# Kernel optimization log

Measured on AMD Instinct MI355X. Metric: run time of the kernel, lower is better.

Reference implementation:

```python
import jax, jax.numpy as jnp
import numpy as np

B, T = 2, 1023
C, H, HS, L, FF = 1024, 16, 64, 6, 4096
V, BS = 50258, 1024


def setup_inputs() -> dict:
    key = jax.random.key(0)
    ks = iter(jax.random.split(key, 80))
    def w(shape):
        return 0.02 * jax.random.normal(next(ks), shape, dtype=jnp.float32)
    inp = {}
    inp['x'] = jax.random.randint(next(ks), (B, T), 0, V)
    inp['y'] = jax.random.randint(next(ks), (B, T), 0, V)
    inp['wte'] = w((V, C))
    inp['wpe_x'] = w((BS, C))
    inp['wpe_y'] = w((BS, C))
    # encoder blocks (stacked over L layers)
    inp['enc_Wq'] = w((L, H, C, HS)); inp['enc_Wk'] = w((L, H, C, HS)); inp['enc_Wv'] = w((L, H, C, HS))
    inp['enc_pw'] = w((L, C, C)); inp['enc_pb'] = jnp.zeros((L, C), jnp.float32)
    inp['enc_ln1g'] = jnp.ones((L, C), jnp.float32); inp['enc_ln1b'] = jnp.zeros((L, C), jnp.float32)
    inp['enc_ln2g'] = jnp.ones((L, C), jnp.float32); inp['enc_ln2b'] = jnp.zeros((L, C), jnp.float32)
    inp['enc_w1'] = w((L, C, FF)); inp['enc_b1'] = jnp.zeros((L, FF), jnp.float32)
    inp['enc_w2'] = w((L, FF, C)); inp['enc_b2'] = jnp.zeros((L, C), jnp.float32)
    # decoder blocks: self-attn (masked), cross-attn, ffn
    inp['dec_sWq'] = w((L, H, C, HS)); inp['dec_sWk'] = w((L, H, C, HS)); inp['dec_sWv'] = w((L, H, C, HS))
    inp['dec_spw'] = w((L, C, C)); inp['dec_spb'] = jnp.zeros((L, C), jnp.float32)
    inp['dec_cWq'] = w((L, H, C, HS)); inp['dec_cWk'] = w((L, H, C, HS)); inp['dec_cWv'] = w((L, H, C, HS))
    inp['dec_cpw'] = w((L, C, C)); inp['dec_cpb'] = jnp.zeros((L, C), jnp.float32)
    inp['dec_ln1g'] = jnp.ones((L, C), jnp.float32); inp['dec_ln1b'] = jnp.zeros((L, C), jnp.float32)
    inp['dec_ln2g'] = jnp.ones((L, C), jnp.float32); inp['dec_ln2b'] = jnp.zeros((L, C), jnp.float32)
    inp['dec_ln3g'] = jnp.ones((L, C), jnp.float32); inp['dec_ln3b'] = jnp.zeros((L, C), jnp.float32)
    inp['dec_w1'] = w((L, C, FF)); inp['dec_b1'] = jnp.zeros((L, FF), jnp.float32)
    inp['dec_w2'] = w((L, FF, C)); inp['dec_b2'] = jnp.zeros((L, C), jnp.float32)
    inp['lnf_g'] = jnp.ones((C,), jnp.float32); inp['lnf_b'] = jnp.zeros((C,), jnp.float32)
    inp['lm_b'] = jnp.zeros((V,), jnp.float32)  # lm_head weight tied to wte
    return inp


def _ln(x, g, b):
    m = x.mean(-1, keepdims=True)
    v = ((x - m) ** 2).mean(-1, keepdims=True)
    return g * (x - m) / jnp.sqrt(v + 1e-5) + b


def _mha(xq, xkv, Wq, Wk, Wv, pw, pb, causal):
    # per-head projections batched over heads: [B,T,C] x [H,C,HS] -> [B,H,T,HS]
    q = jnp.einsum('btc,hcd->bhtd', xq, Wq)
    k = jnp.einsum('bsc,hcd->bhsd', xkv, Wk)
    v = jnp.einsum('bsc,hcd->bhsd', xkv, Wv)
    # NOTE: original scales by sqrt(n_embed) (C from x.size()), not sqrt(head_size)
    s = jnp.einsum('bhtd,bhsd->bhts', q, k) / jnp.sqrt(jnp.float32(C))
    if causal:
        mask = jnp.tril(jnp.ones((xq.shape[1], xkv.shape[1]), bool))
        s = jnp.where(mask, s, -jnp.inf)
    a = jax.nn.softmax(s, axis=-1)
    o = jnp.einsum('bhts,bhsd->bhtd', a, v)
    o = o.transpose(0, 2, 1, 3).reshape(xq.shape[0], xq.shape[1], H * HS)
    return o @ pw + pb


def _ffn(x, w1, b1, w2, b2):
    return jnp.maximum(x @ w1 + b1, 0.0) @ w2 + b2


def _forward(x, y, p):
    enc = p['wte'][x] + p['wpe_x'][:x.shape[1]]
    for i in range(L):
        enc = enc + _ln(_mha(enc, enc, p['enc_Wq'][i], p['enc_Wk'][i], p['enc_Wv'][i], p['enc_pw'][i], p['enc_pb'][i], False), p['enc_ln1g'][i], p['enc_ln1b'][i])
        enc = enc + _ln(_ffn(enc, p['enc_w1'][i], p['enc_b1'][i], p['enc_w2'][i], p['enc_b2'][i]), p['enc_ln2g'][i], p['enc_ln2b'][i])
    dec = p['wte'][y] + p['wpe_y'][:y.shape[1]]
    for i in range(L):
        dec = dec + _ln(_mha(dec, dec, p['dec_sWq'][i], p['dec_sWk'][i], p['dec_sWv'][i], p['dec_spw'][i], p['dec_spb'][i], True), p['dec_ln1g'][i], p['dec_ln1b'][i])
        dec = dec + _ln(_mha(dec, enc, p['dec_cWq'][i], p['dec_cWk'][i], p['dec_cWv'][i], p['dec_cpw'][i], p['dec_cpb'][i], False), p['dec_ln2g'][i], p['dec_ln2b'][i])
        dec = dec + _ln(_ffn(dec, p['dec_w1'][i], p['dec_b1'][i], p['dec_w2'][i], p['dec_b2'][i]), p['dec_ln3g'][i], p['dec_ln3b'][i])
    dec = _ln(dec, p['lnf_g'], p['lnf_b'])
    return dec @ p['wte'].T + p['lm_b']


def reference(x, y, wte, wpe_x, wpe_y,
              enc_Wq, enc_Wk, enc_Wv, enc_pw, enc_pb, enc_ln1g, enc_ln1b, enc_ln2g, enc_ln2b,
              enc_w1, enc_b1, enc_w2, enc_b2,
              dec_sWq, dec_sWk, dec_sWv, dec_spw, dec_spb,
              dec_cWq, dec_cWk, dec_cWv, dec_cpw, dec_cpb,
              dec_ln1g, dec_ln1b, dec_ln2g, dec_ln2b, dec_ln3g, dec_ln3b,
              dec_w1, dec_b1, dec_w2, dec_b2,
              lnf_g, lnf_b, lm_b):
    p = dict(wte=wte, wpe_x=wpe_x, wpe_y=wpe_y,
             enc_Wq=enc_Wq, enc_Wk=enc_Wk, enc_Wv=enc_Wv, enc_pw=enc_pw, enc_pb=enc_pb,
             enc_ln1g=enc_ln1g, enc_ln1b=enc_ln1b, enc_ln2g=enc_ln2g, enc_ln2b=enc_ln2b,
             enc_w1=enc_w1, enc_b1=enc_b1, enc_w2=enc_w2, enc_b2=enc_b2,
             dec_sWq=dec_sWq, dec_sWk=dec_sWk, dec_sWv=dec_sWv, dec_spw=dec_spw, dec_spb=dec_spb,
             dec_cWq=dec_cWq, dec_cWk=dec_cWk, dec_cWv=dec_cWv, dec_cpw=dec_cpw, dec_cpb=dec_cpb,
             dec_ln1g=dec_ln1g, dec_ln1b=dec_ln1b, dec_ln2g=dec_ln2g, dec_ln2b=dec_ln2b,
             dec_ln3g=dec_ln3g, dec_ln3b=dec_ln3b,
             dec_w1=dec_w1, dec_b1=dec_b1, dec_w2=dec_w2, dec_b2=dec_b2,
             lnf_g=lnf_g, lnf_b=lnf_b, lm_b=lm_b)
    return _forward(x, y, p)
```

## Files before the change

### kernel.cpp

```cpp
#include <hip/hip_runtime.h>
#include <hip/hip_bf16.h>

#define BB 2
#define TT 1023
#define CC 1024
#define HH 16
#define HSZ 64
#define LL 6
#define FFD 4096
#define VV 50258
#define MM (BB*TT)
#define MP 2048
#define VP 50304

typedef __attribute__((ext_vector_type(4))) float  f32x4;
typedef __attribute__((ext_vector_type(8))) short  s16x8;
typedef __attribute__((ext_vector_type(4))) short  s16x4;

#define SCHED0   __builtin_amdgcn_sched_barrier(0)
#define SBAR     __builtin_amdgcn_s_barrier()
#define LGKMCNT0 asm volatile("s_waitcnt lgkmcnt(0)" ::: "memory")

__device__ __forceinline__ short f2b(float x) {
    __hip_bfloat16 h = __float2bfloat16(x);
    short s;
    __builtin_memcpy(&s, &h, 2);
    return s;
}
__device__ __forceinline__ float b2f(short s) {
    unsigned u = ((unsigned)(unsigned short)s) << 16;
    float f;
    __builtin_memcpy(&f, &u, 4);
    return f;
}

__device__ __forceinline__ void gld16(const void* g, void* l) {
    __builtin_amdgcn_global_load_lds(
        (__attribute__((address_space(1))) const void*)g,
        (__attribute__((address_space(3))) void*)l, 16, 0, 0);
}

__global__ __launch_bounds__(256) void embed_kernel(
    const int* __restrict__ ids, const float* __restrict__ wte,
    const float* __restrict__ wpe, float* __restrict__ out,
    __hip_bfloat16* __restrict__ outb)
{
    int r = blockIdx.x;
    int t = r % TT;
    long id = ids[r];
    int c = threadIdx.x * 4;
    float4 a = *(const float4*)(wte + id * (long)CC + c);
    float4 p = *(const float4*)(wpe + (long)t * CC + c);
    float4 o; o.x = a.x + p.x; o.y = a.y + p.y; o.z = a.z + p.z; o.w = a.w + p.w;
    *(float4*)(out + (long)r * CC + c) = o;
    s16x4 h; h[0] = f2b(o.x); h[1] = f2b(o.y); h[2] = f2b(o.z); h[3] = f2b(o.w);
    *(s16x4*)(outb + (long)r * CC + c) = h;
}

__global__ __launch_bounds__(256) void cvtb_kernel(
    const float* __restrict__ in, __hip_bfloat16* __restrict__ out, long n)
{
    long i = ((long)blockIdx.x * 256 + threadIdx.x) * 8;
    if (i >= n) return;
    float4 f0 = *(const float4*)(in + i);
    float4 f1 = *(const float4*)(in + i + 4);
    s16x8 h;
    h[0]=f2b(f0.x); h[1]=f2b(f0.y); h[2]=f2b(f0.z); h[3]=f2b(f0.w);
    h[4]=f2b(f1.x); h[5]=f2b(f1.y); h[6]=f2b(f1.z); h[7]=f2b(f1.w);
    *(s16x8*)(out + i) = h;
}

__global__ __launch_bounds__(256) void tcvt_kernel(
    const float* __restrict__ in, __hip_bfloat16* __restrict__ out,
    int R, int S, long inZ, long outZa, long outZb, int zdiv)
{
    int z = blockIdx.z;
    in  += (long)z * inZ;
    out += (long)(z / zdiv) * outZa + (long)(z % zdiv) * outZb;
    __shared__ float tile[32][33];
    int s0 = blockIdx.x * 32, r0 = blockIdx.y * 32;
    int tx = threadIdx.x, ty = threadIdx.y;
    #pragma unroll
    for (int i = 0; i < 4; ++i)
        tile[ty + i * 8][tx] = in[(long)(r0 + ty + i * 8) * S + s0 + tx];
    __syncthreads();
    #pragma unroll
    for (int i = 0; i < 4; ++i)
        out[(long)(s0 + ty + i * 8) * R + r0 + tx] =
            __float2bfloat16(tile[tx][ty + i * 8]);
}

template<int WMODE, bool RELU, int BM, int BN>
__global__ __launch_bounds__(256) void mgemm2_kernel(
    const __hip_bfloat16* __restrict__ A, const __hip_bfloat16* __restrict__ B,
    const float* __restrict__ bias, float* __restrict__ Cm,
    __hip_bfloat16* __restrict__ Cb,
    int M, int N, int K, int ldc, int GM)
{
    constexpr int ASZ  = BM * 32;
    constexpr int BSZ  = BN * 32;
    constexpr int BUF  = ASZ + BSZ;
    constexpr int WROW = BM / 2;
    constexpr int WCOL = BN / 2;
    constexpr int NI   = WROW / 16;
    constexpr int NJ   = WCOL / 16;
    constexpr int NAC  = BM / 64;
    constexpr int NBC  = BN / 64;
    constexpr int L    = NAC + NBC;
    __shared__ short LDS[3 * BUF];

    const int nwg = gridDim.x;
    const int bid = blockIdx.x;
    const int q = nwg >> 3, r = nwg & 7;
    const int xcd = bid & 7, lid = bid >> 3;
    const int swz = (xcd < r) ? xcd * (q + 1) + lid
                              : r * (q + 1) + (xcd - r) * q + lid;
    const int m0 = (swz % GM) * BM;
    const int n0 = (swz / GM) * BN;

    const int tid  = threadIdx.x;
    const int lane = tid & 63, w = tid >> 6;
    const int wr = w >> 1, wc = w & 1;
    const int lr = lane & 15, kg = lane >> 4;

    const __hip_bfloat16* Abase = A + (long)m0 * K;
    const __hip_bfloat16* Bbase = B + (long)n0 * K;

    f32x4 acc[NI][NJ];
    #pragma unroll
    for (int i = 0; i < NI; ++i)
        #pragma unroll
        for (int j = 0; j < NJ; ++j)
            acc[i][j] = (f32x4){0.f, 0.f, 0.f, 0.f};

    const int srow = lane >> 2;
    const int scol = (((lane & 3) ^ ((lane >> 3) & 3))) * 8;

    auto stage = [&](int db, long kofs) {
        short* Ad = &LDS[db * BUF];
        short* Bd = Ad + ASZ;
        #pragma unroll
        for (int p = 0; p < NAC; ++p) {
            int cc = p * 4 + w;
            long ro = (long)(cc * 16 + srow) * K + kofs + scol;
            gld16(Abase + ro, Ad + cc * 512);
        }
        #pragma unroll
        for (int p = 0; p < NBC; ++p) {
            int cc = p * 4 + w;
            long ro = (long)(cc * 16 + srow) * K + kofs + scol;
            gld16(Bbase + ro, Bd + cc * 512);
        }
    };
    const int rslot = (kg ^ ((lr >> 1) & 3)) * 8;

    auto compute = [&](int db) {
        const short* Ar = &LDS[db * BUF];
        const short* Br = Ar + ASZ;
        s16x8 af[NI], bf[NJ];
        #pragma unroll
        for (int i = 0; i < NI; ++i)
            af[i] = *(const s16x8*)&Ar[(wr * WROW + i * 16 + lr) * 32 + rslot];
        #pragma unroll
        for (int j = 0; j < NJ; ++j)
            bf[j] = *(const s16x8*)&Br[(wc * WCOL + j * 16 + lr) * 32 + rslot];
        __builtin_amdgcn_s_setprio(1);
        #pragma unroll
        for (int i = 0; i < NI; ++i)
            #pragma unroll
            for (int j = 0; j < NJ; ++j)
                acc[i][j] = __builtin_amdgcn_mfma_f32_16x16x32_bf16(
                    af[i], bf[j], acc[i][j], 0, 0, 0);
        __builtin_amdgcn_s_setprio(0);
    };

    const int nt = K >> 5;
    stage(0, 0);
    if (nt > 1) stage(1, 32);
    int db = 0;
    for (int t = 0; t < nt; ++t) {
        if (t + 2 < nt) {
            stage((db + 2) % 3, (long)(t + 2) << 5);
            SCHED0;
            if constexpr (L == 4) asm volatile("s_waitcnt vmcnt(8)" ::: "memory");
            else asm volatile("s_waitcnt vmcnt(6)" ::: "memory");
            SCHED0;
        } else if (t + 1 < nt) {
            SCHED0;
            if constexpr (L == 4) asm volatile("s_waitcnt vmcnt(4)" ::: "memory");
            else asm volatile("s_waitcnt vmcnt(3)" ::: "memory");
            SCHED0;
        } else {
            SCHED0; asm volatile("s_waitcnt vmcnt(0)" ::: "memory"); SCHED0;
        }
        SBAR; SCHED0;
        compute(db);
        SCHED0; LGKMCNT0; SCHED0; SBAR; SCHED0;
        db = (db + 1) % 3;
    }

    if (WMODE == 0) {
        float* LF = (float*)&LDS[0];
        if (BM == 128) {
            #pragma unroll
            for (int h = 0; h < 2; ++h) {
                if (wc == h) {
                    #pragma unroll
                    for (int j = 0; j < NJ; ++j) {
                        int gcol = n0 + h * WCOL + j * 16 + lr;
                        float bv = (bias && gcol < N) ? bias[gcol] : 0.f;
                        #pragma unroll
                        for (int i = 0; i < NI; ++i) {
                            int row0 = wr * WROW + i * 16 + kg * 4;
                            #pragma unroll
                            for (int qq = 0; qq < 4; ++qq) {
                                float v = acc[i][j][qq] + bv;
                                if (RELU) v = fmaxf(v, 0.f);
                                LF[(row0 + qq) * 64 + j * 16 + lr] = v;
                            }
                        }
                    }
                }
                __syncthreads();
                #pragma unroll
                for (int i = 0; i < 16; ++i) {
                    int F = i * 256 + tid;
                    int row = F >> 5, col = (F & 31) * 2;
                    int gr = m0 + row, gc = n0 + h * 64 + col;
                    if (gr < M && gc < N)
                        *(float2*)(Cm + (long)gr * ldc + gc) = *(const float2*)&LF[row * 64 + col];
                }
                __syncthreads();
            }
        } else {
            #pragma unroll
            for (int j = 0; j < NJ; ++j) {
                int gcol = n0 + wc * WCOL + j * 16 + lr;
                float bv = (bias && gcol < N) ? bias[gcol] : 0.f;
                #pragma unroll
                for (int i = 0; i < NI; ++i) {
                    int row0 = wr * WROW + i * 16 + kg * 4;
                    #pragma unroll
                    for (int qq = 0; qq < 4; ++qq) {
                        float v = acc[i][j][qq] + bv;
                        if (RELU) v = fmaxf(v, 0.f);
                        LF[(row0 + qq) * BN + wc * WCOL + j * 16 + lr] = v;
                    }
                }
            }
            __syncthreads();
            #pragma unroll
            for (int i = 0; i < BM * BN / 512; ++i) {
                int F = i * 256 + tid;
                int row = F / (BN / 2), col = (F % (BN / 2)) * 2;
                int gr = m0 + row, gc = n0 + col;
                if (gr < M && gc < N)
                    *(float2*)(Cm + (long)gr * ldc + gc) = *(const float2*)&LF[row * BN + col];
            }
        }
    } else {
        short* LS = (short*)&LDS[0];
        #pragma unroll
        for (int j = 0; j < NJ; ++j) {
            int gcol = n0 + wc * WCOL + j * 16 + lr;
            float bv = (bias && gcol < N) ? bias[gcol] : 0.f;
            #pragma unroll
            for (int i = 0; i < NI; ++i) {
                int row0 = wr * WROW + i * 16 + kg * 4;
                #pragma unroll
                for (int qq = 0; qq < 4; ++qq) {
                    float v = acc[i][j][qq] + bv;
                    if (RELU) v = fmaxf(v, 0.f);
                    LS[(row0 + qq) * BN + wc * WCOL + j * 16 + lr] = f2b(v);
                }
            }
        }
        __syncthreads();
        #pragma unroll
        for (int i = 0; i < BM * BN / 2048; ++i) {
            int F = i * 256 + tid;
            int row = F / (BN / 8), col = (F % (BN / 8)) * 8;
            int gr = m0 + row, gc = n0 + col;
            if (gr < M && gc < N)
                *(s16x8*)((short*)Cb + (long)gr * ldc + gc) = *(const s16x8*)&LS[row * BN + col];
        }
    }
}

__global__ __launch_bounds__(256) void mgemm_f32b_kernel(
    const float* __restrict__ A, const float* __restrict__ Bv,
    const float* __restrict__ bias, float* __restrict__ Cm,
    int M, int N, int K, int ldc)
{
    __shared__ short As[128][40];
    __shared__ short Bs[128][40];
    const int tid  = threadIdx.x;
    const int lane = tid & 63, w = tid >> 6;
    const int wr = w >> 1, wc = w & 1;
    const int lr = lane & 15, kg = lane >> 4;
    const int m0 = blockIdx.y * 128, n0 = blockIdx.x * 128;
    const int ar = tid >> 3, ac = (tid & 7) * 4;
    const int br = tid >> 2, bc = (tid & 3) * 8;

    f32x4 acc[4][4];
    #pragma unroll
    for (int i = 0; i < 4; ++i)
        #pragma unroll
        for (int j = 0; j < 4; ++j)
            acc[i][j] = (f32x4){0.f, 0.f, 0.f, 0.f};

    for (int k0 = 0; k0 < K; k0 += 32) {
        #pragma unroll
        for (int p = 0; p < 4; ++p) {
            int row = ar + p * 32, gm = m0 + row;
            float4 f = {0.f, 0.f, 0.f, 0.f};
            if (gm < M) f = *(const float4*)(A + (long)gm * K + k0 + ac);
            s16x4 h; h[0] = f2b(f.x); h[1] = f2b(f.y); h[2] = f2b(f.z); h[3] = f2b(f.w);
            *(s16x4*)&As[row][ac] = h;
        }
        #pragma unroll
        for (int p = 0; p < 2; ++p) {
            int n = br + p * 64, gn = n0 + n;
            s16x8 h = (s16x8){0,0,0,0,0,0,0,0};
            if (gn < N) {
                float4 f0 = *(const float4*)(Bv + (long)gn * K + k0 + bc);
                float4 f1 = *(const float4*)(Bv + (long)gn * K + k0 + bc + 4);
                h[0]=f2b(f0.x); h[1]=f2b(f0.y); h[2]=f2b(f0.z); h[3]=f2b(f0.w);
                h[4]=f2b(f1.x); h[5]=f2b(f1.y); h[6]=f2b(f1.z); h[7]=f2b(f1.w);
            }
            *(s16x8*)&Bs[n][bc] = h;
        }
        __syncthreads();
        s16x8 af[4], bf[4];
        #pragma unroll
        for (int i = 0; i < 4; ++i) af[i] = *(const s16x8*)&As[wr*64 + i*16 + lr][kg*8];
        #pragma unroll
        for (int j = 0; j < 4; ++j) bf[j] = *(const s16x8*)&Bs[wc*64 + j*16 + lr][kg*8];
        #pragma unroll
        for (int i = 0; i < 4; ++i)
            #pragma unroll
            for (int j = 0; j < 4; ++j)
                acc[i][j] = __builtin_amdgcn_mfma_f32_16x16x32_bf16(af[i], bf[j], acc[i][j], 0, 0, 0);
        __syncthreads();
    }
    #pragma unroll
    for (int j = 0; j < 4; ++j) {
        int gcol = n0 + wc * 64 + j * 16 + lr;
        if (gcol >= N) continue;
        float bv = bias ? bias[gcol] : 0.f;
        #pragma unroll
        for (int i = 0; i < 4; ++i) {
            int grow0 = m0 + wr * 64 + i * 16 + kg * 4;
            #pragma unroll
            for (int qq = 0; qq < 4; ++qq) {
                int gr = grow0 + qq;
                if (gr >= M) continue;
                Cm[(long)gr * ldc + gcol] = acc[i][j][qq] + bv;
            }
        }
    }
}

template<bool CAUSAL>
__global__ __launch_bounds__(256) void fattn_kernel(
    const __hip_bfloat16* __restrict__ qkvb, __hip_bfloat16* __restrict__ outb)
{
    __shared__ short Ks[128][72];
    __shared__ short Vt[64][136];
    __shared__ short Ps[4][16][136];

    const int q0 = blockIdx.x * 64;
    const int h = blockIdx.y, b = blockIdx.z;
    const int tid = threadIdx.x;
    const int lane = tid & 63, w = tid >> 6;
    const int lr = lane & 15, lg = lane >> 4;

    const long base = (long)b * TT * 3072;
    const __hip_bfloat16* Kg = qkvb + base + 1024 + h * 64;
    const __hip_bfloat16* Vg = qkvb + base + 2048 + h * 64;

    s16x8 qf[2];
    {
        int qr = q0 + w * 16 + lr;
        #pragma unroll
        for (int kc = 0; kc < 2; ++kc) {
            s16x8 hv = (s16x8){0,0,0,0,0,0,0,0};
            if (qr < TT) {
                hv = *(const s16x8*)(qkvb + base + (long)qr * 3072 + h * 64 + kc * 32 + lg * 8);
                #pragma unroll
                for (int e = 0; e < 8; ++e)
                    hv[e] = f2b(b2f(hv[e]) * 0.03125f);
            }
            qf[kc] = hv;
        }
    }

    f32x4 acc[4];
    #pragma unroll
    for (int jd = 0; jd < 4; ++jd) acc[jd] = (f32x4){0.f, 0.f, 0.f, 0.f};
    float mrun[4] = {-3.0e38f, -3.0e38f, -3.0e38f, -3.0e38f};
    float lrun[4] = {0.f, 0.f, 0.f, 0.f};

    const int send = CAUSAL ? min(TT, q0 + 64) : TT;
    const int nt = (send + 127) >> 7;
    const int sr4 = (tid >> 3) * 4;
    const int dcc = (tid & 7) * 8;

    s16x8 kreg[4], vreg[4];
    auto loadkv = [&](int t) {
        int sbase = t * 128;
        #pragma unroll
        for (int rr = 0; rr < 4; ++rr) {
            int sg = sbase + sr4 + rr;
            if (sg < TT) {
                kreg[rr] = *(const s16x8*)(Kg + (long)sg * 3072 + dcc);
                vreg[rr] = *(const s16x8*)(Vg + (long)sg * 3072 + dcc);
            } else {
                kreg[rr] = (s16x8){0,0,0,0,0,0,0,0};
                vreg[rr] = (s16x8){0,0,0,0,0,0,0,0};
            }
        }
    };

    loadkv(0);
    for (int ti = 0; ti < nt; ++ti) {
        const int s0 = ti * 128;
        SCHED0; SBAR; SCHED0;
        #pragma unroll
        for (int rr = 0; rr < 4; ++rr)
            *(s16x8*)&Ks[sr4 + rr][dcc] = kreg[rr];
        #pragma unroll
        for (int pr = 0; pr < 2; ++pr) {
            #pragma unroll
            for (int e = 0; e < 8; ++e) {
                unsigned pack = (unsigned)(unsigned short)vreg[2*pr][e]
                              | ((unsigned)(unsigned short)vreg[2*pr + 1][e] << 16);
                *(unsigned*)&Vt[dcc + e][sr4 + 2*pr] = pack;
            }
        }
        if (ti + 1 < nt) loadkv(ti + 1);
        SCHED0; LGKMCNT0; SCHED0; SBAR; SCHED0;

        f32x4 sf[8];
        __builtin_amdgcn_s_setprio(1);
        #pragma unroll
        for (int j = 0; j < 8; ++j) {
            f32x4 z = (f32x4){0.f, 0.f, 0.f, 0.f};
            #pragma unroll
            for (int kc = 0; kc < 2; ++kc) {
                s16x8 kf = *(const s16x8*)&Ks[j * 16 + lr][kc * 32 + lg * 8];
                z = __builtin_amdgcn_mfma_f32_16x16x32_bf16(qf[kc], kf, z, 0, 0, 0);
            }
            sf[j] = z;
        }
        __builtin_amdgcn_s_setprio(0);

        float mloc[4] = {-3.0e38f, -3.0e38f, -3.0e38f, -3.0e38f};
        #pragma unroll
        for (int j = 0; j < 8; ++j) {
            int sg = s0 + j * 16 + lr;
            #pragma unroll
            for (int r = 0; r < 4; ++r) {
                float sc = sf[j][r];
                int qg = q0 + w * 16 + lg * 4 + r;
                if ((CAUSAL && sg > qg) || sg >= TT) sc = -3.0e38f;
                sf[j][r] = sc;
                mloc[r] = fmaxf(mloc[r], sc);
            }
        }
        #pragma unroll
        for (int r = 0; r < 4; ++r)
            #pragma unroll
            for (int off = 1; off < 16; off <<= 1)
                mloc[r] = fmaxf(mloc[r], __shfl_xor(mloc[r], off));

        bool grow = false;
        #pragma unroll
        for (int r = 0; r < 4; ++r)
            grow = grow || (mloc[r] > mrun[r] + 8.0f);
        if (__any((int)grow)) {
            #pragma unroll
            for (int r = 0; r < 4; ++r) {
                float mn = fmaxf(mrun[r], mloc[r]);
                float corr = __expf(mrun[r] - mn);
                mrun[r] = mn;
                lrun[r] *= corr;
                #pragma unroll
                for (int jd = 0; jd < 4; ++jd) acc[jd][r] *= corr;
            }
        }

        float psum[4] = {0.f, 0.f, 0.f, 0.f};
        #pragma unroll
        for (int j = 0; j < 8; ++j) {
            #pragma unroll
            for (int r = 0; r < 4; ++r) {
                float p = __expf(sf[j][r] - mrun[r]);
                psum[r] += p;
                Ps[w][lg * 4 + r][j * 16 + lr] = f2b(p);
            }
        }
        #pragma unroll
        for (int r = 0; r < 4; ++r) {
            #pragma unroll
            for (int off = 1; off < 16; off <<= 1)
                psum[r] += __shfl_xor(psum[r], off);
            lrun[r] += psum[r];
        }

        __builtin_amdgcn_s_setprio(1);
        #pragma unroll
        for (int kc = 0; kc < 4; ++kc) {
            s16x8 pa = *(const s16x8*)&Ps[w][lr][kc * 32 + lg * 8];
            #pragma unroll
            for (int jd = 0; jd < 4; ++jd) {
                s16x8 bv = *(const s16x8*)&Vt[jd * 16 + lr][kc * 32 + lg * 8];
                acc[jd] = __builtin_amdgcn_mfma_f32_16x16x32_bf16(pa, bv, acc[jd], 0, 0, 0);
            }
        }
        __builtin_amdgcn_s_setprio(0);
        SCHED0; LGKMCNT0; SCHED0;
    }

    #pragma unroll
    for (int r = 0; r < 4; ++r) {
        int qg = q0 + w * 16 + lg * 4 + r;
        if (qg >= TT) continue;
        float inv = 1.0f / lrun[r];
        #pragma unroll
        for (int jd = 0; jd < 4; ++jd)
            outb[((long)b * TT + qg) * CC + h * 64 + jd * 16 + lr] =
                __float2bfloat16(acc[jd][r] * inv);
    }
}

__global__ __launch_bounds__(256) void ln_kernel(
    const float* __restrict__ in, const float* __restrict__ res,
    const float* __restrict__ g, const float* __restrict__ b,
    float* __restrict__ out, __hip_bfloat16* __restrict__ outb)
{
    const int r = blockIdx.x, tid = threadIdx.x;
    __shared__ float sm[4];

    float4 xv = *(const float4*)(in + (long)r * CC + tid * 4);
    float s = xv.x + xv.y + xv.z + xv.w;
    #pragma unroll
    for (int o = 32; o > 0; o >>= 1) s += __shfl_xor(s, o);
    if ((tid & 63) == 0) sm[tid >> 6] = s;
    __syncthreads();
    const float mean = (sm[0] + sm[1] + sm[2] + sm[3]) * (1.0f / CC);
    __syncthreads();

    float4 d; d.x = xv.x - mean; d.y = xv.y - mean; d.z = xv.z - mean; d.w = xv.w - mean;
    float s2 = d.x * d.x + d.y * d.y + d.z * d.z + d.w * d.w;
    #pragma unroll
    for (int o = 32; o > 0; o >>= 1) s2 += __shfl_xor(s2, o);
    if ((tid & 63) == 0) sm[tid >> 6] = s2;
    __syncthreads();
    const float rstd = rsqrtf((sm[0] + sm[1] + sm[2] + sm[3]) * (1.0f / CC) + 1e-5f);

    float4 gv = *(const float4*)(g + tid * 4);
    float4 bv = *(const float4*)(b + tid * 4);
    float4 o;
    o.x = gv.x * d.x * rstd + bv.x; o.y = gv.y * d.y * rstd + bv.y;
    o.z = gv.z * d.z * rstd + bv.z; o.w = gv.w * d.w * rstd + bv.w;
    if (res) {
        float4 rv = *(const float4*)(res + (long)r * CC + tid * 4);
        o.x += rv.x; o.y += rv.y; o.z += rv.z; o.w += rv.w;
    }
    if (out) *(float4*)(out + (long)r * CC + tid * 4) = o;
    if (outb) {
        s16x4 h; h[0] = f2b(o.x); h[1] = f2b(o.y); h[2] = f2b(o.z); h[3] = f2b(o.w);
        *(s16x4*)(outb + (long)r * CC + tid * 4) = h;
    }
}

__global__ __launch_bounds__(256) void lnb_kernel(
    const __hip_bfloat16* __restrict__ in, const float* __restrict__ res,
    const float* __restrict__ g, const float* __restrict__ b,
    float* __restrict__ out, __hip_bfloat16* __restrict__ outb)
{
    const int r = blockIdx.x, tid = threadIdx.x;
    __shared__ float sm[4];

    s16x4 hv = *(const s16x4*)((const short*)in + (long)r * CC + tid * 4);
    float4 xv;
    xv.x = b2f(hv[0]); xv.y = b2f(hv[1]); xv.z = b2f(hv[2]); xv.w = b2f(hv[3]);
    float s = xv.x + xv.y + xv.z + xv.w;
    #pragma unroll
    for (int o = 32; o > 0; o >>= 1) s += __shfl_xor(s, o);
    if ((tid & 63) == 0) sm[tid >> 6] = s;
    __syncthreads();
    const float mean = (sm[0] + sm[1] + sm[2] + sm[3]) * (1.0f / CC);
    __syncthreads();

    float4 d; d.x = xv.x - mean; d.y = xv.y - mean; d.z = xv.z - mean; d.w = xv.w - mean;
    float s2 = d.x * d.x + d.y * d.y + d.z * d.z + d.w * d.w;
    #pragma unroll
    for (int o = 32; o > 0; o >>= 1) s2 += __shfl_xor(s2, o);
    if ((tid & 63) == 0) sm[tid >> 6] = s2;
    __syncthreads();
    const float rstd = rsqrtf((sm[0] + sm[1] + sm[2] + sm[3]) * (1.0f / CC) + 1e-5f);

    float4 gv = *(const float4*)(g + tid * 4);
    float4 bv = *(const float4*)(b + tid * 4);
    float4 o;
    o.x = gv.x * d.x * rstd + bv.x; o.y = gv.y * d.y * rstd + bv.y;
    o.z = gv.z * d.z * rstd + bv.z; o.w = gv.w * d.w * rstd + bv.w;
    if (res) {
        float4 rv = *(const float4*)(res + (long)r * CC + tid * 4);
        o.x += rv.x; o.y += rv.y; o.z += rv.z; o.w += rv.w;
    }
    *(float4*)(out + (long)r * CC + tid * 4) = o;
    s16x4 hh; hh[0] = f2b(o.x); hh[1] = f2b(o.y); hh[2] = f2b(o.z); hh[3] = f2b(o.w);
    *(s16x4*)((short*)outb + (long)r * CC + tid * 4) = hh;
}

extern "C" void kernel_launch(void* const* d_in, const int* in_sizes, int n_in,
                              void* d_out, int out_size, void* d_ws, size_t ws_size,
                              hipStream_t stream)
{
    const int*   x      = (const int*)  d_in[0];
    const int*   y      = (const int*)  d_in[1];
    const float* wte    = (const float*)d_in[2];
    const float* wpe_x  = (const float*)d_in[3];
    const float* wpe_y  = (const float*)d_in[4];
    const float* eWq    = (const float*)d_in[5];
    const float* eWk    = (const float*)d_in[6];
    const float* eWv    = (const float*)d_in[7];
    const float* epw    = (const float*)d_in[8];
    const float* epb    = (const float*)d_in[9];
    const float* eln1g  = (const float*)d_in[10];
    const float* eln1b  = (const float*)d_in[11];
    const float* eln2g  = (const float*)d_in[12];
    const float* eln2b  = (const float*)d_in[13];
    const float* ew1    = (const float*)d_in[14];
    const float* eb1    = (const float*)d_in[15];
    const float* ew2    = (const float*)d_in[16];
    const float* eb2    = (const float*)d_in[17];
    const float* dsWq   = (const float*)d_in[18];
    const float* dsWk   = (const float*)d_in[19];
    const float* dsWv   = (const float*)d_in[20];
    const float* dspw   = (const float*)d_in[21];
    const float* dspb   = (const float*)d_in[22];
    const float* dcWq   = (const float*)d_in[23];
    const float* dcWk   = (const float*)d_in[24];
    const float* dcWv   = (const float*)d_in[25];
    const float* dcpw   = (const float*)d_in[26];
    const float* dcpb   = (const float*)d_in[27];
    const float* dln1g  = (const float*)d_in[28];
    const float* dln1b  = (const float*)d_in[29];
    const float* dln2g  = (const float*)d_in[30];
    const float* dln2b  = (const float*)d_in[31];
    const float* dln3g  = (const float*)d_in[32];
    const float* dln3b  = (const float*)d_in[33];
    const float* dw1    = (const float*)d_in[34];
    const float* db1    = (const float*)d_in[35];
    const float* dw2    = (const float*)d_in[36];
    const float* db2    = (const float*)d_in[37];
    const float* lnfg   = (const float*)d_in[38];
    const float* lnfb   = (const float*)d_in[39];
    const float* lm_b   = (const float*)d_in[40];

    float* out = (float*)d_out;

    const size_t MCp = (size_t)MP * CC;
    float* enc = (float*)d_ws;
    float* dec = enc + MCp;
    float* t0  = dec + MCp;
    __hip_bfloat16* encb = (__hip_bfloat16*)(t0 + MCp);
    __hip_bfloat16* decb = encb + MCp;
    __hip_bfloat16* t0b  = decb + MCp;
    __hip_bfloat16* a0b  = t0b + MCp;
    __hip_bfloat16* qkvb = a0b + MCp;
    __hip_bfloat16* ffb  = qkvb + (size_t)MP * 3072;
    __hip_bfloat16* wteb = ffb + (size_t)MP * FFD;
    __hip_bfloat16* eQKVw = wteb + (size_t)VP * CC;
    __hip_bfloat16* ePWw  = eQKVw + (size_t)LL * 3072 * CC;
    __hip_bfloat16* eW1w  = ePWw  + (size_t)LL * CC * CC;
    __hip_bfloat16* eW2w  = eW1w  + (size_t)LL * FFD * CC;
    __hip_bfloat16* sQKVw = eW2w  + (size_t)LL * CC * FFD;
    __hip_bfloat16* sPWw  = sQKVw + (size_t)LL * 3072 * CC;
    __hip_bfloat16* cQKVw = sPWw  + (size_t)LL * CC * CC;
    __hip_bfloat16* cPWw  = cQKVw + (size_t)LL * 3072 * CC;
    __hip_bfloat16* dW1w  = cPWw  + (size_t)LL * CC * CC;
    __hip_bfloat16* dW2w  = dW1w  + (size_t)LL * FFD * CC;
    __hip_bfloat16* bigEnd = dW2w + (size_t)LL * CC * FFD;
    __hip_bfloat16* wb = eQKVw;
    const size_t needBig   = (size_t)((char*)bigEnd - (char*)d_ws);
    const size_t needSmall = (size_t)((char*)(wb + (size_t)FFD * CC) - (char*)d_ws);
    const size_t needWteb  = (size_t)((char*)eQKVw - (char*)d_ws);
    const bool big     = (ws_size >= needBig);
    const bool useWteb = (ws_size >= needWteb) &&
                         (big || ws_size >= needSmall);

    const int QT = (TT + 63) / 64;
    const dim3 tblk(32, 8);

    auto gemm = [&](const __hip_bfloat16* A, const __hip_bfloat16* B,
                    const float* bias, __hip_bfloat16* Cb,
                    int N_, int K_, int ldc, bool relu) {
        if (N_ <= 2048) {
            const int GMv = MP / 64;
            int nwg = GMv * ((N_ + 127) / 128);
            if (relu) mgemm2_kernel<2, true , 64, 128><<<nwg, 256, 0, stream>>>(A, B, bias, nullptr, Cb, MM, N_, K_, ldc, GMv);
            else      mgemm2_kernel<2, false, 64, 128><<<nwg, 256, 0, stream>>>(A, B, bias, nullptr, Cb, MM, N_, K_, ldc, GMv);
        } else {
            const int GMv = MP / 128;
            int nwg = GMv * ((N_ + 127) / 128);
            if (relu) mgemm2_kernel<2, true , 128, 128><<<nwg, 256, 0, stream>>>(A, B, bias, nullptr, Cb, MM, N_, K_, ldc, GMv);
            else      mgemm2_kernel<2, false, 128, 128><<<nwg, 256, 0, stream>>>(A, B, bias, nullptr, Cb, MM, N_, K_, ldc, GMv);
        }
    };

    if (useWteb) {
        long n = (long)VV * CC;
        cvtb_kernel<<<(int)((n / 8 + 255) / 256), 256, 0, stream>>>(wte, wteb, n);
    }

    if (big) {
        const long sWH = (long)CC * HSZ;
        const long oA = (long)3072 * CC;
        const long oB = (long)HSZ * CC;
        dim3 gq(HSZ / 32, CC / 32, LL * HH);
        tcvt_kernel<<<gq, tblk, 0, stream>>>(eWq, eQKVw,             CC, HSZ, sWH, oA, oB, HH);
        tcvt_kernel<<<gq, tblk, 0, stream>>>(eWk, eQKVw + CC * CC,   CC, HSZ, sWH, oA, oB, HH);
        tcvt_kernel<<<gq, tblk, 0, stream>>>(eWv, eQKVw + 2*CC*CC,   CC, HSZ, sWH, oA, oB, HH);
        tcvt_kernel<<<gq, tblk, 0, stream>>>(dsWq, sQKVw,            CC, HSZ, sWH, oA, oB, HH);
        tcvt_kernel<<<gq, tblk, 0, stream>>>(dsWk, sQKVw + CC * CC,  CC, HSZ, sWH, oA, oB, HH);
        tcvt_kernel<<<gq, tblk, 0, stream>>>(dsWv, sQKVw + 2*CC*CC,  CC, HSZ, sWH, oA, oB, HH);
        tcvt_kernel<<<gq, tblk, 0, stream>>>(dcWq, cQKVw,            CC, HSZ, sWH, oA, oB, HH);
        tcvt_kernel<<<gq, tblk, 0, stream>>>(dcWk, cQKVw + CC * CC,  CC, HSZ, sWH, oA, oB, HH);
        tcvt_kernel<<<gq, tblk, 0, stream>>>(dcWv, cQKVw + 2*CC*CC,  CC, HSZ, sWH, oA, oB, HH);
        dim3 gp(CC / 32, CC / 32, LL);
        tcvt_kernel<<<gp, tblk, 0, stream>>>(epw,  ePWw, CC, CC, (long)CC*CC, (long)CC*CC, 0, 1);
        tcvt_kernel<<<gp, tblk, 0, stream>>>(dspw, sPWw, CC, CC, (long)CC*CC, (long)CC*CC, 0, 1);
        tcvt_kernel<<<gp, tblk, 0, stream>>>(dcpw, cPWw, CC, CC, (long)CC*CC, (long)CC*CC, 0, 1);
        dim3 g1(FFD / 32, CC / 32, LL);
        tcvt_kernel<<<g1, tblk, 0, stream>>>(ew1, eW1w, CC, FFD, (long)CC*FFD, (long)FFD*CC, 0, 1);
        tcvt_kernel<<<g1, tblk, 0, stream>>>(dw1, dW1w, CC, FFD, (long)CC*FFD, (long)FFD*CC, 0, 1);
        dim3 g2(CC / 32, FFD / 32, LL);
        tcvt_kernel<<<g2, tblk, 0, stream>>>(ew2, eW2w, FFD, CC, (long)FFD*CC, (long)CC*FFD, 0, 1);
        tcvt_kernel<<<g2, tblk, 0, stream>>>(dw2, dW2w, FFD, CC, (long)FFD*CC, (long)CC*FFD, 0, 1);
    }

    auto cvt_qkv = [&](const float* Wq, const float* Wk, const float* Wv) {
        dim3 g(HSZ / 32, CC / 32, HH);
        tcvt_kernel<<<g, tblk, 0, stream>>>(Wq, wb,             CC, HSZ, (long)CC*HSZ, (long)HSZ*CC, 0, 1);
        tcvt_kernel<<<g, tblk, 0, stream>>>(Wk, wb + CC*CC,     CC, HSZ, (long)CC*HSZ, (long)HSZ*CC, 0, 1);
        tcvt_kernel<<<g, tblk, 0, stream>>>(Wv, wb + 2*CC*CC,   CC, HSZ, (long)CC*HSZ, (long)HSZ*CC, 0, 1);
    };
    auto cvt_nt = [&](const float* W, int R, int S) {
        dim3 g(S / 32, R / 32, 1);
        tcvt_kernel<<<g, tblk, 0, stream>>>(W, wb, R, S, 0, 0, 0, 1);
    };

    embed_kernel<<<MM, 256, 0, stream>>>(x, wte, wpe_x, enc, encb);
    for (int i = 0; i < LL; ++i) {
        const long cOff = (long)i * CC;
        const __hip_bfloat16 *Wqkv, *Wp, *W1, *W2;
        if (big) {
            Wqkv = eQKVw + (size_t)i * 3072 * CC;
            Wp   = ePWw  + (size_t)i * CC * CC;
            W1   = eW1w  + (size_t)i * FFD * CC;
            W2   = eW2w  + (size_t)i * CC * FFD;
        }
        if (!big) cvt_qkv(eWq + (long)i*HH*CC*HSZ, eWk + (long)i*HH*CC*HSZ, eWv + (long)i*HH*CC*HSZ), Wqkv = wb;
        gemm(encb, Wqkv, nullptr, qkvb, 3072, CC, 3072, false);
        fattn_kernel<false><<<dim3(QT, HH, BB), 256, 0, stream>>>(qkvb, a0b);
        if (!big) cvt_nt(epw + (long)i*CC*CC, CC, CC), Wp = wb;
        gemm(a0b, Wp, epb + cOff, t0b, CC, CC, CC, false);
        lnb_kernel<<<MM, 256, 0, stream>>>(t0b, enc, eln1g + cOff, eln1b + cOff, enc, encb);
        if (!big) cvt_nt(ew1 + (long)i*CC*FFD, CC, FFD), W1 = wb;
        gemm(encb, W1, eb1 + (long)i*FFD, ffb, FFD, CC, FFD, true);
        if (!big) cvt_nt(ew2 + (long)i*FFD*CC, FFD, CC), W2 = wb;
        gemm(ffb, W2, eb2 + cOff, t0b, CC, FFD, CC, false);
        lnb_kernel<<<MM, 256, 0, stream>>>(t0b, enc, eln2g + cOff, eln2b + cOff, enc, encb);
    }

    embed_kernel<<<MM, 256, 0, stream>>>(y, wte, wpe_y, dec, decb);
    for (int i = 0; i < LL; ++i) {
        const long cOff = (long)i * CC;
        const __hip_bfloat16 *Ws, *Wsp, *Wc, *Wcp, *W1, *W2;
        if (big) {
            Ws  = sQKVw + (size_t)i * 3072 * CC;
            Wsp = sPWw  + (size_t)i * CC * CC;
            Wc  = cQKVw + (size_t)i * 3072 * CC;
            Wcp = cPWw  + (size_t)i * CC * CC;
            W1  = dW1w  + (size_t)i * FFD * CC;
            W2  = dW2w  + (size_t)i * CC * FFD;
        }
        if (!big) cvt_qkv(dsWq + (long)i*HH*CC*HSZ, dsWk + (long)i*HH*CC*HSZ, dsWv + (long)i*HH*CC*HSZ), Ws = wb;
        gemm(decb, Ws, nullptr, qkvb, 3072, CC, 3072, false);
        fattn_kernel<true><<<dim3(QT, HH, BB), 256, 0, stream>>>(qkvb, a0b);
        if (!big) cvt_nt(dspw + (long)i*CC*CC, CC, CC), Wsp = wb;
        gemm(a0b, Wsp, dspb + cOff, t0b, CC, CC, CC, false);
        lnb_kernel<<<MM, 256, 0, stream>>>(t0b, dec, dln1g + cOff, dln1b + cOff, dec, decb);
        if (!big) cvt_qkv(dcWq + (long)i*HH*CC*HSZ, dcWk + (long)i*HH*CC*HSZ, dcWv + (long)i*HH*CC*HSZ), Wc = wb;
        gemm(decb, Wc, nullptr, qkvb, CC, CC, 3072, false);
        gemm(encb, Wc + (size_t)CC * CC, nullptr, qkvb + CC, 2048, CC, 3072, false);
        fattn_kernel<false><<<dim3(QT, HH, BB), 256, 0, stream>>>(qkvb, a0b);
        if (!big) cvt_nt(dcpw + (long)i*CC*CC, CC, CC), Wcp = wb;
        gemm(a0b, Wcp, dcpb + cOff, t0b, CC, CC, CC, false);
        lnb_kernel<<<MM, 256, 0, stream>>>(t0b, dec, dln2g + cOff, dln2b + cOff, dec, decb);
        if (!big) cvt_nt(dw1 + (long)i*CC*FFD, CC, FFD), W1 = wb;
        gemm(decb, W1, db1 + (long)i*FFD, ffb, FFD, CC, FFD, true);
        if (!big) cvt_nt(dw2 + (long)i*FFD*CC, FFD, CC), W2 = wb;
        gemm(ffb, W2, db2 + cOff, t0b, CC, FFD, CC, false);
        lnb_kernel<<<MM, 256, 0, stream>>>(t0b, dec, dln3g + cOff, dln3b + cOff, dec, decb);
    }

    ln_kernel<<<MM, 256, 0, stream>>>(dec, nullptr, lnfg, lnfb,
                                      useWteb ? nullptr : t0, t0b);
    if (useWteb) {
        const int GMv = 1024 / 128;
        const int nwg = GMv * ((VV + 127) / 128);
        mgemm2_kernel<0, false, 128, 128><<<nwg, 256, 0, stream>>>(
            t0b, wteb, lm_b, out, nullptr, 1024, VV, CC, VV, GMv);
        mgemm2_kernel<0, false, 128, 128><<<nwg, 256, 0, stream>>>(
            t0b + (size_t)1024 * CC, wteb, lm_b, out + (size_t)1024 * VV, nullptr,
            MM - 1024, VV, CC, VV, GMv);
    } else {
        dim3 grid((VV + 127) / 128, MP / 128);
        mgemm_f32b_kernel<<<grid, 256, 0, stream>>>(t0, wte, lm_b, out, MM, VV, CC, VV);
    }
}
```

Before: 3.090 ms.

## Split-K the N=1024 projection and FFN-down GEMMs, summing halves in layernorm

The output projection and FFN second GEMMs (N=1024) now run with a 2-way split over K. Each half writes a bf16 partial to its own buffer, and the bias is added only by the first half. The following layernorm kernel reads both partials and adds them before normalizing. This doubles the workgroup count on these small-N GEMMs to fill more compute units, at the cost of an extra bf16 intermediate write/read and bf16 rounding of each partial.

```diff
diff --git a/kernel.cpp b/kernel.cpp
--- a/kernel.cpp
+++ b/kernel.cpp
@@ -90,12 +90,12 @@
             __float2bfloat16(tile[tx][ty + i * 8]);
 }
 
-template<int WMODE, bool RELU, int BM, int BN>
+template<int WMODE, bool RELU, int BM, int BN, bool SPLITK>
 __global__ __launch_bounds__(256) void mgemm2_kernel(
     const __hip_bfloat16* __restrict__ A, const __hip_bfloat16* __restrict__ B,
     const float* __restrict__ bias, float* __restrict__ Cm,
-    __hip_bfloat16* __restrict__ Cb,
-    int M, int N, int K, int ldc, int GM)
+    __hip_bfloat16* __restrict__ Cb, __hip_bfloat16* __restrict__ Cb2,
+    int M, int N, int K, int Kstride, int ldc, int GM)
 {
     constexpr int ASZ  = BM * 32;
     constexpr int BSZ  = BN * 32;
@@ -113,8 +113,14 @@
     const int bid = blockIdx.x;
     const int q = nwg >> 3, r = nwg & 7;
     const int xcd = bid & 7, lid = bid >> 3;
-    const int swz = (xcd < r) ? xcd * (q + 1) + lid
-                              : r * (q + 1) + (xcd - r) * q + lid;
+    int swz = (xcd < r) ? xcd * (q + 1) + lid
+                        : r * (q + 1) + (xcd - r) * q + lid;
+    int ks = 0;
+    if (SPLITK) {
+        const int hN = nwg >> 1;
+        ks = (swz >= hN);
+        swz -= ks * hN;
+    }
     const int m0 = (swz % GM) * BM;
     const int n0 = (swz / GM) * BN;
 
@@ -123,8 +129,10 @@
     const int wr = w >> 1, wc = w & 1;
     const int lr = lane & 15, kg = lane >> 4;
 
-    const __hip_bfloat16* Abase = A + (long)m0 * K;
-    const __hip_bfloat16* Bbase = B + (long)n0 * K;
+    const __hip_bfloat16* Abase = A + (long)m0 * Kstride + (SPLITK ? ks * K : 0);
+    const __hip_bfloat16* Bbase = B + (long)n0 * Kstride + (SPLITK ? ks * K : 0);
+    const float* biasU = (SPLITK && ks) ? nullptr : bias;
+    __hip_bfloat16* CbU = (SPLITK && ks) ? Cb2 : Cb;
 
     f32x4 acc[NI][NJ];
     #pragma unroll
@@ -142,13 +150,13 @@
         #pragma unroll
         for (int p = 0; p < NAC; ++p) {
             int cc = p * 4 + w;
-            long ro = (long)(cc * 16 + srow) * K + kofs + scol;
+            long ro = (long)(cc * 16 + srow) * Kstride + kofs + scol;
             gld16(Abase + ro, Ad + cc * 512);
         }
         #pragma unroll
         for (int p = 0; p < NBC; ++p) {
             int cc = p * 4 + w;
-            long ro = (long)(cc * 16 + srow) * K + kofs + scol;
+            long ro = (long)(cc * 16 + srow) * Kstride + kofs + scol;
             gld16(Bbase + ro, Bd + cc * 512);
         }
     };
@@ -208,7 +216,7 @@
                     #pragma unroll
                     for (int j = 0; j < NJ; ++j) {
                         int gcol = n0 + h * WCOL + j * 16 + lr;
-                        float bv = (bias && gcol < N) ? bias[gcol] : 0.f;
+                        float bv = (biasU && gcol < N) ? biasU[gcol] : 0.f;
                         #pragma unroll
                         for (int i = 0; i < NI; ++i) {
                             int row0 = wr * WROW + i * 16 + kg * 4;
@@ -236,7 +244,7 @@
             #pragma unroll
             for (int j = 0; j < NJ; ++j) {
                 int gcol = n0 + wc * WCOL + j * 16 + lr;
-                float bv = (bias && gcol < N) ? bias[gcol] : 0.f;
+                float bv = (biasU && gcol < N) ? biasU[gcol] : 0.f;
                 #pragma unroll
                 for (int i = 0; i < NI; ++i) {
                     int row0 = wr * WROW + i * 16 + kg * 4;
@@ -263,7 +271,7 @@
         #pragma unroll
         for (int j = 0; j < NJ; ++j) {
             int gcol = n0 + wc * WCOL + j * 16 + lr;
-            float bv = (bias && gcol < N) ? bias[gcol] : 0.f;
+            float bv = (biasU && gcol < N) ? biasU[gcol] : 0.f;
             #pragma unroll
             for (int i = 0; i < NI; ++i) {
                 int row0 = wr * WROW + i * 16 + kg * 4;
@@ -282,7 +290,7 @@
             int row = F / (BN / 8), col = (F % (BN / 8)) * 8;
             int gr = m0 + row, gc = n0 + col;
             if (gr < M && gc < N)
-                *(s16x8*)((short*)Cb + (long)gr * ldc + gc) = *(const s16x8*)&LS[row * BN + col];
+                *(s16x8*)((short*)CbU + (long)gr * ldc + gc) = *(const s16x8*)&LS[row * BN + col];
         }
     }
 }
@@ -576,7 +584,8 @@
 }
 
 __global__ __launch_bounds__(256) void lnb_kernel(
-    const __hip_bfloat16* __restrict__ in, const float* __restrict__ res,
+    const __hip_bfloat16* __restrict__ in, const __hip_bfloat16* __restrict__ in2,
+    const float* __restrict__ res,
     const float* __restrict__ g, const float* __restrict__ b,
     float* __restrict__ out, __hip_bfloat16* __restrict__ outb)
 {
@@ -586,6 +595,10 @@
     s16x4 hv = *(const s16x4*)((const short*)in + (long)r * CC + tid * 4);
     float4 xv;
     xv.x = b2f(hv[0]); xv.y = b2f(hv[1]); xv.z = b2f(hv[2]); xv.w = b2f(hv[3]);
+    if (in2) {
+        s16x4 h2 = *(const s16x4*)((const short*)in2 + (long)r * CC + tid * 4);
+        xv.x += b2f(h2[0]); xv.y += b2f(h2[1]); xv.z += b2f(h2[2]); xv.w += b2f(h2[3]);
+    }
     float s = xv.x + xv.y + xv.z + xv.w;
     #pragma unroll
     for (int o = 32; o > 0; o >>= 1) s += __shfl_xor(s, o);
@@ -671,7 +684,8 @@
     __hip_bfloat16* encb = (__hip_bfloat16*)(t0 + MCp);
     __hip_bfloat16* decb = encb + MCp;
     __hip_bfloat16* t0b  = decb + MCp;
-    __hip_bfloat16* a0b  = t0b + MCp;
+    __hip_bfloat16* t0c  = t0b + MCp;
+    __hip_bfloat16* a0b  = t0c + MCp;
     __hip_bfloat16* qkvb = a0b + MCp;
     __hip_bfloat16* ffb  = qkvb + (size_t)MP * 3072;
     __hip_bfloat16* wteb = ffb + (size_t)MP * FFD;
@@ -703,14 +717,21 @@
         if (N_ <= 2048) {
             const int GMv = MP / 64;
             int nwg = GMv * ((N_ + 127) / 128);
-            if (relu) mgemm2_kernel<2, true , 64, 128><<<nwg, 256, 0, stream>>>(A, B, bias, nullptr, Cb, MM, N_, K_, ldc, GMv);
-            else      mgemm2_kernel<2, false, 64, 128><<<nwg, 256, 0, stream>>>(A, B, bias, nullptr, Cb, MM, N_, K_, ldc, GMv);
+            if (relu) mgemm2_kernel<2, true , 64, 128, false><<<nwg, 256, 0, stream>>>(A, B, bias, nullptr, Cb, nullptr, MM, N_, K_, K_, ldc, GMv);
+            else      mgemm2_kernel<2, false, 64, 128, false><<<nwg, 256, 0, stream>>>(A, B, bias, nullptr, Cb, nullptr, MM, N_, K_, K_, ldc, GMv);
         } else {
             const int GMv = MP / 128;
             int nwg = GMv * ((N_ + 127) / 128);
-            if (relu) mgemm2_kernel<2, true , 128, 128><<<nwg, 256, 0, stream>>>(A, B, bias, nullptr, Cb, MM, N_, K_, ldc, GMv);
-            else      mgemm2_kernel<2, false, 128, 128><<<nwg, 256, 0, stream>>>(A, B, bias, nullptr, Cb, MM, N_, K_, ldc, GMv);
-        }
+            if (relu) mgemm2_kernel<2, true , 128, 128, false><<<nwg, 256, 0, stream>>>(A, B, bias, nullptr, Cb, nullptr, MM, N_, K_, K_, ldc, GMv);
+            else      mgemm2_kernel<2, false, 128, 128, false><<<nwg, 256, 0, stream>>>(A, B, bias, nullptr, Cb, nullptr, MM, N_, K_, K_, ldc, GMv);
+        }
+    };
+    auto gemm_sk = [&](const __hip_bfloat16* A, const __hip_bfloat16* B,
+                       const float* bias, int K_) {
+        const int GMv = MP / 64;
+        int nwg = 2 * GMv * (CC / 128);
+        mgemm2_kernel<2, false, 64, 128, true><<<nwg, 256, 0, stream>>>(
+            A, B, bias, nullptr, t0b, t0c, MM, CC, K_ / 2, K_, CC, GMv);
     };
 
     if (useWteb) {
@@ -769,13 +790,13 @@
         gemm(encb, Wqkv, nullptr, qkvb, 3072, CC, 3072, false);
         fattn_kernel<false><<<dim3(QT, HH, BB), 256, 0, stream>>>(qkvb, a0b);
         if (!big) cvt_nt(epw + (long)i*CC*CC, CC, CC), Wp = wb;
-        gemm(a0b, Wp, epb + cOff, t0b, CC, CC, CC, false);
-        lnb_kernel<<<MM, 256, 0, stream>>>(t0b, enc, eln1g + cOff, eln1b + cOff, enc, encb);
+        gemm_sk(a0b, Wp, epb + cOff, CC);
+        lnb_kernel<<<MM, 256, 0, stream>>>(t0b, t0c, enc, eln1g + cOff, eln1b + cOff, enc, encb);
         if (!big) cvt_nt(ew1 + (long)i*CC*FFD, CC, FFD), W1 = wb;
         gemm(encb, W1, eb1 + (long)i*FFD, ffb, FFD, CC, FFD, true);
         if (!big) cvt_nt(ew2 + (long)i*FFD*CC, FFD, CC), W2 = wb;
-        gemm(ffb, W2, eb2 + cOff, t0b, CC, FFD, CC, false);
-        lnb_kernel<<<MM, 256, 0, stream>>>(t0b, enc, eln2g + cOff, eln2b + cOff, enc, encb);
+        gemm_sk(ffb, W2, eb2 + cOff, FFD);
+        lnb_kernel<<<MM, 256, 0, stream>>>(t0b, t0c, enc, eln2g + cOff, eln2b + cOff, enc, encb);
     }
 
     embed_kernel<<<MM, 256, 0, stream>>>(y, wte, wpe_y, dec, decb);
@@ -794,20 +815,20 @@
         gemm(decb, Ws, nullptr, qkvb, 3072, CC, 3072, false);
         fattn_kernel<true><<<dim3(QT, HH, BB), 256, 0, stream>>>(qkvb, a0b);
         if (!big) cvt_nt(dspw + (long)i*CC*CC, CC, CC), Wsp = wb;
-        gemm(a0b, Wsp, dspb + cOff, t0b, CC, CC, CC, false);
-        lnb_kernel<<<MM, 256, 0, stream>>>(t0b, dec, dln1g + cOff, dln1b + cOff, dec, decb);
+        gemm_sk(a0b, Wsp, dspb + cOff, CC);
+        lnb_kernel<<<MM, 256, 0, stream>>>(t0b, t0c, dec, dln1g + cOff, dln1b + cOff, dec, decb);
         if (!big) cvt_qkv(dcWq + (long)i*HH*CC*HSZ, dcWk + (long)i*HH*CC*HSZ, dcWv + (long)i*HH*CC*HSZ), Wc = wb;
         gemm(decb, Wc, nullptr, qkvb, CC, CC, 3072, false);
         gemm(encb, Wc + (size_t)CC * CC, nullptr, qkvb + CC, 2048, CC, 3072, false);
         fattn_kernel<false><<<dim3(QT, HH, BB), 256, 0, stream>>>(qkvb, a0b);
         if (!big) cvt_nt(dcpw + (long)i*CC*CC, CC, CC), Wcp = wb;
-        gemm(a0b, Wcp, dcpb + cOff, t0b, CC, CC, CC, false);
-        lnb_kernel<<<MM, 256, 0, stream>>>(t0b, dec, dln2g + cOff, dln2b + cOff, dec, decb);
+        gemm_sk(a0b, Wcp, dcpb + cOff, CC);
+        lnb_kernel<<<MM, 256, 0, stream>>>(t0b, t0c, dec, dln2g + cOff, dln2b + cOff, dec, decb);
         if (!big) cvt_nt(dw1 + (long)i*CC*FFD, CC, FFD), W1 = wb;
         gemm(decb, W1, db1 + (long)i*FFD, ffb, FFD, CC, FFD, true);
         if (!big) cvt_nt(dw2 + (long)i*FFD*CC, FFD, CC), W2 = wb;
-        gemm(ffb, W2, db2 + cOff, t0b, CC, FFD, CC, false);
-        lnb_kernel<<<MM, 256, 0, stream>>>(t0b, dec, dln3g + cOff, dln3b + cOff, dec, decb);
+        gemm_sk(ffb, W2, db2 + cOff, FFD);
+        lnb_kernel<<<MM, 256, 0, stream>>>(t0b, t0c, dec, dln3g + cOff, dln3b + cOff, dec, decb);
     }
 
     ln_kernel<<<MM, 256, 0, stream>>>(dec, nullptr, lnfg, lnfb,
@@ -815,11 +836,11 @@
     if (useWteb) {
         const int GMv = 1024 / 128;
         const int nwg = GMv * ((VV + 127) / 128);
-        mgemm2_kernel<0, false, 128, 128><<<nwg, 256, 0, stream>>>(
-            t0b, wteb, lm_b, out, nullptr, 1024, VV, CC, VV, GMv);
-        mgemm2_kernel<0, false, 128, 128><<<nwg, 256, 0, stream>>>(
-            t0b + (size_t)1024 * CC, wteb, lm_b, out + (size_t)1024 * VV, nullptr,
-            MM - 1024, VV, CC, VV, GMv);
+        mgemm2_kernel<0, false, 128, 128, false><<<nwg, 256, 0, stream>>>(
+            t0b, wteb, lm_b, out, nullptr, nullptr, 1024, VV, CC, CC, VV, GMv);
+        mgemm2_kernel<0, false, 128, 128, false><<<nwg, 256, 0, stream>>>(
+            t0b + (size_t)1024 * CC, wteb, lm_b, out + (size_t)1024 * VV, nullptr, nullptr,
+            MM - 1024, VV, CC, CC, VV, GMv);
     } else {
         dim3 grid((VV + 127) / 128, MP / 128);
         mgemm_f32b_kernel<<<grid, 256, 0, stream>>>(t0, wte, lm_b, out, MM, VV, CC, VV);
```

Result: faster. 2.993 ms (-3.1%).
